# Performance work log

Measured on AMD Instinct MI355X. Metric: run time of the kernel, lower is better.

## Reference

```python
import jax, jax.numpy as jnp
import numpy as np

STATE_DIM = 8
SLOT_DIM = 128
B, T, K = 128, 6, 64


def _mlp(x, w1, b1, w2, b2):
    return jax.nn.relu(x @ w1 + b1) @ w2 + b2


def setup_inputs() -> dict:
    key = jax.random.key(0)
    ks = jax.random.split(key, 24)
    s = 0.02
    def w(k, shape):
        return jax.random.normal(k, shape, dtype=jnp.float32) * s
    D, H = STATE_DIM, SLOT_DIM
    return {
        "gt_states": jax.random.normal(ks[0], (B, T, K, D), dtype=jnp.float32),
        "rollout_steps": 5,
        "enc_w1": w(ks[1], (D, H)),  "enc_b1": jnp.zeros((H,), jnp.float32),
        "enc_w2": w(ks[2], (H, H)),  "enc_b2": jnp.zeros((H,), jnp.float32),
        "self_w1": w(ks[3], (H, H)), "self_b1": jnp.zeros((H,), jnp.float32),
        "self_w2": w(ks[4], (H, H)), "self_b2": jnp.zeros((H,), jnp.float32),
        "inter_w1": w(ks[5], (2 * H, H)), "inter_b1": jnp.zeros((H,), jnp.float32),
        "inter_w2": w(ks[6], (H, H)),     "inter_b2": jnp.zeros((H,), jnp.float32),
        "upd_w1": w(ks[7], (2 * H, H)), "upd_b1": jnp.zeros((H,), jnp.float32),
        "upd_w2": w(ks[8], (H, H)),     "upd_b2": jnp.zeros((H,), jnp.float32),
        "dec_w1": w(ks[9], (H, H)),  "dec_b1": jnp.zeros((H,), jnp.float32),
        "dec_w2": w(ks[10], (H, D)), "dec_b2": jnp.zeros((D,), jnp.float32),
    }


def reference(gt_states, rollout_steps, enc_w1, enc_b1, enc_w2, enc_b2,
              self_w1, self_b1, self_w2, self_b2,
              inter_w1, inter_b1, inter_w2, inter_b2,
              upd_w1, upd_b1, upd_w2, upd_b2,
              dec_w1, dec_b1, dec_w2, dec_b2):
    Tn = gt_states.shape[1]
    n_steps = min(Tn - 1, int(rollout_steps))
    H = enc_w1.shape[1]
    # split the concat-MLP first layer: cat([si, sj]) @ W1 == si @ W1a + sj @ W1b
    wi_a, wi_b = inter_w1[:H], inter_w1[H:]

    slots = _mlp(gt_states[:, 0], enc_w1, enc_b1, enc_w2, enc_b2)  # [B,K,H]
    preds = []
    for _ in range(n_steps):
        delta_self = _mlp(slots, self_w1, self_b1, self_w2, self_b2)  # [B,K,H]
        a = slots @ wi_a  # sender (i) contribution, [B,K,H]
        b = slots @ wi_b  # receiver (j) contribution, [B,K,H]
        # pairwise pre-activation [B,K(i),K(j),H]
        pre = a[:, :, None, :] + b[:, None, :, :] + inter_b1
        effects = jax.nn.relu(pre) @ inter_w2 + inter_b2  # [B,K,K,H]
        delta_inter = effects.mean(axis=1)  # mean over i -> [B,K,H]
        slots = _mlp(jnp.concatenate([delta_self, delta_inter], axis=-1),
                     upd_w1, upd_b1, upd_w2, upd_b2)
        pred = _mlp(slots, dec_w1, dec_b1, dec_w2, dec_b2)  # [B,K,D]
        preds.append(pred)
        slots = _mlp(pred, enc_w1, enc_b1, enc_w2, enc_b2)
    pred_states = jnp.stack(preds, axis=1)  # [B,n_steps,K,D]
    target_states = gt_states[:, 1:int(rollout_steps) + 1]
    return pred_states, target_states
```

## Files before the change

### kernel.cpp

```cpp
#include <hip/hip_runtime.h>

#define BB 128
#define TT 6
#define KK 64
#define DD 8
#define HH 128
#define NSTEP 5
#define LDP 136
#define PREDSZ (BB*NSTEP*KK*DD)

typedef unsigned short u16;
typedef unsigned int   u32;
typedef _Float16 f16;
typedef __attribute__((ext_vector_type(8))) _Float16 f16x8;
typedef __attribute__((ext_vector_type(4))) float f32x4;
typedef __attribute__((ext_vector_type(2))) unsigned int u32x2;
typedef __attribute__((ext_vector_type(4))) unsigned int u32x4;
typedef __attribute__((ext_vector_type(2))) _Float16 h2;

union h2u { u32 u; h2 h; };
union hu  { u16 u; f16 h; };

__device__ __forceinline__ u16 f2h_bits(float f){
  hu v; v.h = (f16)f; return v.u;
}
__device__ __forceinline__ u32 pk2(float x, float y){
  hu a, b; a.h = (f16)x; b.h = (f16)y;
  return (u32)a.u | ((u32)b.u << 16);
}
__device__ __forceinline__ h2 u2h(u32 x){ h2u t; t.u = x; return t.h; }
__device__ __forceinline__ u32 h2u_(h2 x){ h2u t; t.h = x; return t.u; }

#define O_EWA   0
#define O_EWB   16384
#define O_EWS   32768
#define O_SUIU  49152
#define O_UD    81920
#define O_DET   98304
#define O_DW2T  114688
#define BIASF   57856

template<bool RELU>
__device__ __forceinline__ void gemmJ(const u16 (*A)[LDP], const u16* __restrict__ wt,
    float bias, u16 (*O)[LDP], int wn, int wm, int l15, int q, int n, int lane)
{
  f16x8 bf[4];
#pragma unroll
  for (int kc=0; kc<4; ++kc)
    bf[kc] = *(const f16x8*)(wt + (wn<<11) + (kc<<9) + (lane<<3));
#pragma unroll
  for (int mt=0; mt<2; ++mt){
    f32x4 acc = {0.f,0.f,0.f,0.f};
#pragma unroll
    for (int kc=0; kc<4; ++kc){
      f16x8 af = *(const f16x8*)&A[(wm<<5)+(mt<<4)+l15][(kc<<5)+(q<<3)];
      acc = __builtin_amdgcn_mfma_f32_16x16x32_f16(af, bf[kc], acc, 0,0,0);
    }
#pragma unroll
    for (int e=0; e<4; ++e){
      float v = acc[e] + bias;
      if (RELU) v = fmaxf(v, 0.f);
      O[(wm<<5)+(mt<<4)+(q<<2)+e][n] = f2h_bits(v);
    }
  }
}

__device__ __forceinline__ void gemm256J(const u16 (*A1)[LDP], const u16 (*A2)[LDP],
    const u16* __restrict__ wt, float bias, u16 (*O)[LDP], int wn, int wm, int l15, int q, int n, int lane)
{
  f16x8 bf[8];
#pragma unroll
  for (int kc=0; kc<8; ++kc)
    bf[kc] = *(const f16x8*)(wt + (wn<<12) + (kc<<9) + (lane<<3));
#pragma unroll
  for (int mt=0; mt<2; ++mt){
    f32x4 acc = {0.f,0.f,0.f,0.f};
#pragma unroll
    for (int kc=0; kc<8; ++kc){
      const u16 (*As)[LDP] = (kc<4) ? A1 : A2;
      f16x8 af = *(const f16x8*)&As[(wm<<5)+(mt<<4)+l15][((kc&3)<<5)+(q<<3)];
      acc = __builtin_amdgcn_mfma_f32_16x16x32_f16(af, bf[kc], acc, 0,0,0);
    }
#pragma unroll
    for (int e=0; e<4; ++e){
      float v = fmaxf(acc[e] + bias, 0.f);
      O[(wm<<5)+(mt<<4)+(q<<2)+e][n] = f2h_bits(v);
    }
  }
}

__device__ __forceinline__ void fusedS1I(const u16 (*P)[LDP], const u16* __restrict__ ws,
    float bAv, float bBv, float bSv,
    u16 (*Q)[LDP], u16 (*S)[LDP],
    int wn, int wm, int l15, int q, int n, int lane)
{
  f16x8 fa[4], fb[4], fs[4];
#pragma unroll
  for (int kc=0; kc<4; ++kc){
    const int o = (wn<<11) + (kc<<9) + (lane<<3);
    fa[kc] = *(const f16x8*)(ws + O_EWA + o);
    fb[kc] = *(const f16x8*)(ws + O_EWB + o);
    fs[kc] = *(const f16x8*)(ws + O_EWS + o);
  }
  u32 aPk[4][2], bPk[4][2];
#pragma unroll
  for (int mt=0; mt<4; ++mt){
    f16x8 af[4];
#pragma unroll
    for (int kc=0; kc<4; ++kc)
      af[kc] = *(const f16x8*)&P[(mt<<4)+l15][(kc<<5)+(q<<3)];
    f32x4 aA = {0.f,0.f,0.f,0.f}, aB = {0.f,0.f,0.f,0.f};
#pragma unroll
    for (int kc=0; kc<4; ++kc){
      aA = __builtin_amdgcn_mfma_f32_16x16x32_f16(af[kc], fa[kc], aA, 0,0,0);
      aB = __builtin_amdgcn_mfma_f32_16x16x32_f16(af[kc], fb[kc], aB, 0,0,0);
    }
    aPk[mt][0] = pk2(aA[0]+bAv, aA[1]+bAv);
    aPk[mt][1] = pk2(aA[2]+bAv, aA[3]+bAv);
    bPk[mt][0] = pk2(aB[0]+bBv, aB[1]+bBv);
    bPk[mt][1] = pk2(aB[2]+bBv, aB[3]+bBv);
    if ((mt>>1) == wm){
      f32x4 hA = {0.f,0.f,0.f,0.f};
#pragma unroll
      for (int kc=0; kc<4; ++kc)
        hA = __builtin_amdgcn_mfma_f32_16x16x32_f16(af[kc], fs[kc], hA, 0,0,0);
#pragma unroll
      for (int e=0; e<4; ++e)
        S[(mt<<4)+(q<<2)+e][n] = f2h_bits(fmaxf(hA[e]+bSv, 0.f));
    }
  }

  const u32 b0 = bPk[(wm<<1)][0],   b1 = bPk[(wm<<1)][1];
  const u32 b2 = bPk[(wm<<1)+1][0], b3 = bPk[(wm<<1)+1][1];
  u32 jt[4][4];
#pragma unroll
  for (int qp=0; qp<4; ++qp){
    const int src = (qp<<4) + l15;
    jt[qp][0] = (u32)__shfl((int)b0, src);
    jt[qp][1] = (u32)__shfl((int)b1, src);
    jt[qp][2] = (u32)__shfl((int)b2, src);
    jt[qp][3] = (u32)__shfl((int)b3, src);
  }
  h2 z; z.x = (f16)0.f; z.y = (f16)0.f;
  h2 s[4][4];
#pragma unroll
  for (int qp=0; qp<4; ++qp)
#pragma unroll
    for (int X=0; X<4; ++X) s[qp][X] = z;
#pragma unroll
  for (int mt=0; mt<4; ++mt)
#pragma unroll
    for (int p=0; p<2; ++p){
      const u32 ap = aPk[mt][p];
      const h2 hl = u2h(__builtin_amdgcn_perm(ap, ap, 0x01000100));
      const h2 hh = u2h(__builtin_amdgcn_perm(ap, ap, 0x03020302));
#pragma unroll
      for (int qp=0; qp<4; ++qp)
#pragma unroll
        for (int X=0; X<4; ++X){
          const h2 bt = u2h(jt[qp][X]);
          s[qp][X] += __builtin_elementwise_max(hl + bt, z);
          s[qp][X] += __builtin_elementwise_max(hh + bt, z);
        }
    }
#pragma unroll
  for (int m=0; m<2; ++m){
    const int msk = 16 << m;
#pragma unroll
    for (int qp=0; qp<4; ++qp)
#pragma unroll
      for (int X=0; X<4; ++X)
        s[qp][X] += u2h((u32)__shfl_xor((int)h2u_(s[qp][X]), msk));
  }
#pragma unroll
  for (int qp=0; qp<4; ++qp) if (qp == q){
#pragma unroll
    for (int X=0; X<4; ++X){
      const int mh = X>>1, p = X&1;
      const int j = (wm<<5) + (mh<<4) + (qp<<2) + (p<<1);
      hu lo, hi; lo.h = s[qp][X].x; hi.h = s[qp][X].y;
      Q[j][n]   = lo.u;
      Q[j+1][n] = hi.u;
    }
  }
}

__device__ __forceinline__ void dec_out(const u16 (*S)[LDP], const u16* __restrict__ dwt,
    float db2v, float* __restrict__ out, int b, int t, int tid)
{
  const int r = tid>>3, d = tid&7;
  float acc = db2v;
#pragma unroll
  for (int c=0; c<16; ++c){
    f16x8 hv = *(const f16x8*)&S[r][c<<3];
    f16x8 wv = *(const f16x8*)(dwt + (d<<7) + (c<<3));
#pragma unroll
    for (int j=0; j<8; ++j)
      acc += (float)hv[j] * (float)wv[j];
  }
  out[(size_t)(b*NSTEP + t)*(KK*DD) + (r<<3) + d] = acc;
}

__device__ __forceinline__ void mlp_in8(const float* pred, const float* __restrict__ W,
    const float* __restrict__ bias, u16 (*O)[LDP], int tid)
{
  const int h = tid & 127, rg = tid >> 7;
  float wv[DD];
#pragma unroll
  for (int d=0; d<DD; ++d) wv[d] = W[d*HH + h];
  const float bv = bias[h];
  for (int rr=0; rr<8; ++rr){
    const int r = (rg<<3) + rr;
    float v = bv;
#pragma unroll
    for (int d=0; d<DD; ++d) v += pred[r*DD + d] * wv[d];
    O[r][h] = f2h_bits(fmaxf(v, 0.f));
  }
}

__global__ void prep_kernel(
    const float* __restrict__ ew1, const float* __restrict__ eb1,
    const float* __restrict__ ew2, const float* __restrict__ eb2,
    const float* __restrict__ sw1, const float* __restrict__ sb1,
    const float* __restrict__ sw2, const float* __restrict__ sb2,
    const float* __restrict__ iw1, const float* __restrict__ ib1,
    const float* __restrict__ iw2, const float* __restrict__ ib2,
    const float* __restrict__ uw1, const float* __restrict__ ub1,
    const float* __restrict__ uw2, const float* __restrict__ ub2,
    const float* __restrict__ dw1, const float* __restrict__ db1,
    const float* __restrict__ dw2, const float* __restrict__ db2,
    u16* __restrict__ ws)
{
  const int idx = blockIdx.x * 256 + threadIdx.x;
  if (idx < 49152){
    const int mat = idx >> 14, r = idx & 16383;
    const int g = r >> 11, kc = (r >> 9) & 3, lane = (r >> 3) & 63, e = r & 7;
    const int k  = (kc<<5) + ((lane>>4)<<3) + e;
    const int nn = (g<<4) + (lane & 15);
    float v = 0.f;
    if (mat == 0){ for (int m=0; m<HH; ++m) v += ew2[k*HH+m] * iw1[m*HH+nn]; }
    else if (mat == 1){ for (int m=0; m<HH; ++m) v += ew2[k*HH+m] * iw1[(HH+m)*HH+nn]; }
    else { for (int m=0; m<HH; ++m) v += ew2[k*HH+m] * sw1[m*HH+nn]; }
    hu hb; hb.h = (f16)v; ws[idx] = hb.u;
  } else if (idx < 81920){
    const int r = idx - 49152;
    const int g = r >> 12, kc = (r >> 9) & 7, lane = (r >> 3) & 63, e = r & 7;
    const int k  = ((kc&3)<<5) + ((lane>>4)<<3) + e;
    const int nn = (g<<4) + (lane & 15);
    float v = 0.f;
    if (kc < 4){ for (int m=0; m<HH; ++m) v += sw2[k*HH+m] * uw1[m*HH+nn]; }
    else { for (int m=0; m<HH; ++m) v += iw2[k*HH+m] * uw1[(HH+m)*HH+nn]; v *= (1.f/64.f); }
    hu hb; hb.h = (f16)v; ws[idx] = hb.u;
  } else if (idx < 98304){
    const int r = idx - 81920;
    const int g = r >> 11, kc = (r >> 9) & 3, lane = (r >> 3) & 63, e = r & 7;
    const int k  = (kc<<5) + ((lane>>4)<<3) + e;
    const int nn = (g<<4) + (lane & 15);
    float v = 0.f;
    for (int m=0; m<HH; ++m) v += uw2[k*HH+m] * dw1[m*HH+nn];
    hu hb; hb.h = (f16)v; ws[idx] = hb.u;
  } else if (idx < 114688){
    const int r = idx - 98304;
    const int g = r >> 11, kc = (r >> 9) & 3, lane = (r >> 3) & 63, e = r & 7;
    const int k  = (kc<<5) + ((lane>>4)<<3) + e;
    const int nn = (g<<4) + (lane & 15);
    float v = 0.f;
#pragma unroll
    for (int d=0; d<DD; ++d) v += dw2[k*DD+d] * ew1[d*HH+nn];
    hu hb; hb.h = (f16)v; ws[idx] = hb.u;
  } else if (idx < 115712){
    const int r = idx - 114688, d = r >> 7, hcol = r & 127;
    hu hb; hb.h = (f16)dw2[hcol*DD + d]; ws[idx] = hb.u;
  } else if (idx < 116480){
    const int j = idx - 115712, which = j >> 7, nn = j & 127;
    float v = 0.f;
    switch (which){
      case 0: for (int m=0; m<HH; ++m) v += eb2[m] * iw1[m*HH+nn]; break;
      case 1: for (int m=0; m<HH; ++m) v += eb2[m] * iw1[(HH+m)*HH+nn]; v += ib1[nn]; break;
      case 2: for (int m=0; m<HH; ++m) v += eb2[m] * sw1[m*HH+nn]; v += sb1[nn]; break;
      case 3: for (int m=0; m<HH; ++m) v += sb2[m]*uw1[m*HH+nn] + ib2[m]*uw1[(HH+m)*HH+nn];
              v += ub1[nn]; break;
      case 4: for (int m=0; m<HH; ++m) v += ub2[m] * dw1[m*HH+nn]; v += db1[nn]; break;
      default:
#pragma unroll
        for (int d=0; d<DD; ++d) v += db2[d] * ew1[d*HH+nn];
        v += eb1[nn]; break;
    }
    ((float*)ws)[BIASF + j] = v;
  }
}

__global__ __launch_bounds__(1024, 4) void rollout_kernel(
    const float* __restrict__ gt, const int* __restrict__ rollout,
    const float* __restrict__ ew1, const float* __restrict__ eb1,
    const float* __restrict__ db2,
    const u16* __restrict__ ws, float* __restrict__ out)
{
  extern __shared__ u16 smem[];
  u16 (*P)[LDP] = (u16(*)[LDP])smem;
  u16 (*Q)[LDP] = (u16(*)[LDP])(smem + KK*LDP);
  u16 (*R)[LDP] = (u16(*)[LDP])(smem + 2*KK*LDP);
  u16 (*S)[LDP] = (u16(*)[LDP])(smem + 3*KK*LDP);
  float* predbuf = (float*)S;

  const int tid = threadIdx.x, b = blockIdx.x;
  const int w = tid >> 6, lane = tid & 63;
  const int l15 = lane & 15, q = lane >> 4;
  const int wn = w & 7, wm = w >> 3;
  const int n = (wn << 4) + l15;

  int ns = rollout[0];
  if (ns > TT-1) ns = TT-1;
  if (ns > NSTEP) ns = NSTEP;
  if (ns < 0) ns = 0;

  const float* bf32 = (const float*)ws;
  const float bAv  = bf32[BIASF + n];
  const float bBv  = bf32[BIASF + 128 + n];
  const float bSv  = bf32[BIASF + 256 + n];
  const float bUv  = bf32[BIASF + 384 + n];
  const float bUDv = bf32[BIASF + 512 + n];
  const float debv = bf32[BIASF + 640 + n];
  const float db2v = db2[tid & 7];

  for (int i=tid; i<NSTEP*KK*DD; i+=1024)
    out[PREDSZ + b*(NSTEP*KK*DD) + i] = gt[(size_t)b*(TT*KK*DD) + KK*DD + i];
  if (tid < KK*DD) predbuf[tid] = gt[(size_t)b*(TT*KK*DD) + tid];
  __syncthreads();
  mlp_in8(predbuf, ew1, eb1, P, tid);
  __syncthreads();

  for (int t=0; t<ns; ++t){
    fusedS1I(P, ws, bAv, bBv, bSv, Q, S, wn, wm, l15, q, n, lane);
    __syncthreads();
    gemm256J(S, Q, ws+O_SUIU, bUv, R, wn, wm, l15, q, n, lane);
    __syncthreads();
    gemmJ<true>(R, ws+O_UD, bUDv, S, wn, wm, l15, q, n, lane);
    __syncthreads();
    gemmJ<true>(S, ws+O_DET, debv, P, wn, wm, l15, q, n, lane);
    if (tid < 512) dec_out(S, ws+O_DW2T, db2v, out, b, t, tid);
    __syncthreads();
  }
}

extern "C" void kernel_launch(void* const* d_in, const int* in_sizes, int n_in,
                              void* d_out, int out_size, void* d_ws, size_t ws_size,
                              hipStream_t stream)
{
  const float* gt  = (const float*)d_in[0];
  const int*   rs  = (const int*)d_in[1];
  const float* ew1 = (const float*)d_in[2];
  const float* eb1 = (const float*)d_in[3];
  const float* ew2 = (const float*)d_in[4];
  const float* eb2 = (const float*)d_in[5];
  const float* sw1 = (const float*)d_in[6];
  const float* sb1 = (const float*)d_in[7];
  const float* sw2 = (const float*)d_in[8];
  const float* sb2 = (const float*)d_in[9];
  const float* iw1 = (const float*)d_in[10];
  const float* ib1 = (const float*)d_in[11];
  const float* iw2 = (const float*)d_in[12];
  const float* ib2 = (const float*)d_in[13];
  const float* uw1 = (const float*)d_in[14];
  const float* ub1 = (const float*)d_in[15];
  const float* uw2 = (const float*)d_in[16];
  const float* ub2 = (const float*)d_in[17];
  const float* dw1 = (const float*)d_in[18];
  const float* db1 = (const float*)d_in[19];
  const float* dw2 = (const float*)d_in[20];
  const float* db2 = (const float*)d_in[21];
  float* out = (float*)d_out;
  u16*   ws  = (u16*)d_ws;

  const int smem_bytes = 4 * KK * LDP * (int)sizeof(u16);
  (void)hipFuncSetAttribute((const void*)rollout_kernel,
                            hipFuncAttributeMaxDynamicSharedMemorySize, smem_bytes);

  hipLaunchKernelGGL(prep_kernel, dim3(455), dim3(256), 0, stream,
                     ew1, eb1, ew2, eb2, sw1, sb1, sw2, sb2, iw1, ib1, iw2, ib2,
                     uw1, ub1, uw2, ub2, dw1, db1, dw2, db2, ws);
  hipLaunchKernelGGL(rollout_kernel, dim3(BB), dim3(1024), smem_bytes, stream,
                     gt, rs, ew1, eb1, db2, ws, out);
}
```

Baseline: 205.2 us.

## Split each batch across two blocks with global-memory slot exchange per step

Each batch element is now handled by two 512-thread blocks instead of one 1024-thread block, so 256 blocks fill more of the GPU's compute units. Each block computes half the receiver rows and half of the update/decoder rows. After every step the two blocks swap their halves of the new slot matrix through a global workspace buffer, coordinated by release/acquire flags and a spin-wait. This trades more parallelism for an inter-block handshake every step, and both blocks must be co-resident or the wait only ends at the guard limit.

After: 198.3 us. 1.03x faster.

```diff
diff --git a/kernel.cpp b/kernel.cpp
--- a/kernel.cpp
+++ b/kernel.cpp
@@ -39,10 +39,12 @@
 #define O_DET   98304
 #define O_DW2T  114688
 #define BIASF   57856
+#define O_XBUF  131072
+#define O_FLAG  (O_XBUF + 128*2*2*4096)
 
 template<bool RELU>
-__device__ __forceinline__ void gemmJ(const u16 (*A)[LDP], const u16* __restrict__ wt,
-    float bias, u16 (*O)[LDP], int wn, int wm, int l15, int q, int n, int lane)
+__device__ __forceinline__ void gemmH(const u16 (*A)[LDP], const u16* __restrict__ wt,
+    float bias, u16 (*O)[LDP], int wn, int l15, int q, int n, int lane)
 {
   f16x8 bf[4];
 #pragma unroll
@@ -53,20 +55,20 @@
     f32x4 acc = {0.f,0.f,0.f,0.f};
 #pragma unroll
     for (int kc=0; kc<4; ++kc){
-      f16x8 af = *(const f16x8*)&A[(wm<<5)+(mt<<4)+l15][(kc<<5)+(q<<3)];
+      f16x8 af = *(const f16x8*)&A[(mt<<4)+l15][(kc<<5)+(q<<3)];
       acc = __builtin_amdgcn_mfma_f32_16x16x32_f16(af, bf[kc], acc, 0,0,0);
     }
 #pragma unroll
     for (int e=0; e<4; ++e){
       float v = acc[e] + bias;
       if (RELU) v = fmaxf(v, 0.f);
-      O[(wm<<5)+(mt<<4)+(q<<2)+e][n] = f2h_bits(v);
-    }
-  }
-}
-
-__device__ __forceinline__ void gemm256J(const u16 (*A1)[LDP], const u16 (*A2)[LDP],
-    const u16* __restrict__ wt, float bias, u16 (*O)[LDP], int wn, int wm, int l15, int q, int n, int lane)
+      O[(mt<<4)+(q<<2)+e][n] = f2h_bits(v);
+    }
+  }
+}
+
+__device__ __forceinline__ void gemm256H(const u16 (*A1)[LDP], const u16 (*A2)[LDP],
+    const u16* __restrict__ wt, float bias, u16 (*O)[LDP], int wn, int l15, int q, int n, int lane)
 {
   f16x8 bf[8];
 #pragma unroll
@@ -78,13 +80,13 @@
 #pragma unroll
     for (int kc=0; kc<8; ++kc){
       const u16 (*As)[LDP] = (kc<4) ? A1 : A2;
-      f16x8 af = *(const f16x8*)&As[(wm<<5)+(mt<<4)+l15][((kc&3)<<5)+(q<<3)];
+      f16x8 af = *(const f16x8*)&As[(mt<<4)+l15][((kc&3)<<5)+(q<<3)];
       acc = __builtin_amdgcn_mfma_f32_16x16x32_f16(af, bf[kc], acc, 0,0,0);
     }
 #pragma unroll
     for (int e=0; e<4; ++e){
       float v = fmaxf(acc[e] + bias, 0.f);
-      O[(wm<<5)+(mt<<4)+(q<<2)+e][n] = f2h_bits(v);
+      O[(mt<<4)+(q<<2)+e][n] = f2h_bits(v);
     }
   }
 }
@@ -92,7 +94,7 @@
 __device__ __forceinline__ void fusedS1I(const u16 (*P)[LDP], const u16* __restrict__ ws,
     float bAv, float bBv, float bSv,
     u16 (*Q)[LDP], u16 (*S)[LDP],
-    int wn, int wm, int l15, int q, int n, int lane)
+    int wn, int half, int l15, int q, int n, int lane)
 {
   f16x8 fa[4], fb[4], fs[4];
 #pragma unroll
@@ -119,19 +121,19 @@
     aPk[mt][1] = pk2(aA[2]+bAv, aA[3]+bAv);
     bPk[mt][0] = pk2(aB[0]+bBv, aB[1]+bBv);
     bPk[mt][1] = pk2(aB[2]+bBv, aB[3]+bBv);
-    if ((mt>>1) == wm){
+    if ((mt>>1) == half){
       f32x4 hA = {0.f,0.f,0.f,0.f};
 #pragma unroll
       for (int kc=0; kc<4; ++kc)
         hA = __builtin_amdgcn_mfma_f32_16x16x32_f16(af[kc], fs[kc], hA, 0,0,0);
 #pragma unroll
       for (int e=0; e<4; ++e)
-        S[(mt<<4)+(q<<2)+e][n] = f2h_bits(fmaxf(hA[e]+bSv, 0.f));
-    }
-  }
-
-  const u32 b0 = bPk[(wm<<1)][0],   b1 = bPk[(wm<<1)][1];
-  const u32 b2 = bPk[(wm<<1)+1][0], b3 = bPk[(wm<<1)+1][1];
+        S[((mt&1)<<4)+(q<<2)+e][n] = f2h_bits(fmaxf(hA[e]+bSv, 0.f));
+    }
+  }
+
+  const u32 b0 = bPk[(half<<1)][0],   b1 = bPk[(half<<1)][1];
+  const u32 b2 = bPk[(half<<1)+1][0], b3 = bPk[(half<<1)+1][1];
   u32 jt[4][4];
 #pragma unroll
   for (int qp=0; qp<4; ++qp){
@@ -177,7 +179,7 @@
 #pragma unroll
     for (int X=0; X<4; ++X){
       const int mh = X>>1, p = X&1;
-      const int j = (wm<<5) + (mh<<4) + (qp<<2) + (p<<1);
+      const int j = (mh<<4) + (qp<<2) + (p<<1);
       hu lo, hi; lo.h = s[qp][X].x; hi.h = s[qp][X].y;
       Q[j][n]   = lo.u;
       Q[j+1][n] = hi.u;
@@ -186,7 +188,7 @@
 }
 
 __device__ __forceinline__ void dec_out(const u16 (*S)[LDP], const u16* __restrict__ dwt,
-    float db2v, float* __restrict__ out, int b, int t, int tid)
+    float db2v, float* __restrict__ out, int batch, int half, int t, int tid)
 {
   const int r = tid>>3, d = tid&7;
   float acc = db2v;
@@ -198,7 +200,7 @@
     for (int j=0; j<8; ++j)
       acc += (float)hv[j] * (float)wv[j];
   }
-  out[(size_t)(b*NSTEP + t)*(KK*DD) + (r<<3) + d] = acc;
+  out[(size_t)(batch*NSTEP + t)*(KK*DD) + ((half<<5)+r)*DD + d] = acc;
 }
 
 __device__ __forceinline__ void mlp_in8(const float* pred, const float* __restrict__ W,
@@ -209,8 +211,8 @@
 #pragma unroll
   for (int d=0; d<DD; ++d) wv[d] = W[d*HH + h];
   const float bv = bias[h];
-  for (int rr=0; rr<8; ++rr){
-    const int r = (rg<<3) + rr;
+  for (int rr=0; rr<16; ++rr){
+    const int r = (rg<<4) + rr;
     float v = bv;
 #pragma unroll
     for (int d=0; d<DD; ++d) v += pred[r*DD + d] * wv[d];
@@ -232,6 +234,7 @@
     u16* __restrict__ ws)
 {
   const int idx = blockIdx.x * 256 + threadIdx.x;
+  if (idx < 512) ((u32*)(ws + O_FLAG))[idx] = 0;
   if (idx < 49152){
     const int mat = idx >> 14, r = idx & 16383;
     const int g = r >> 11, kc = (r >> 9) & 3, lane = (r >> 3) & 63, e = r & 7;
@@ -290,23 +293,24 @@
   }
 }
 
-__global__ __launch_bounds__(1024, 4) void rollout_kernel(
+__global__ __launch_bounds__(512, 2) void rollout_kernel(
     const float* __restrict__ gt, const int* __restrict__ rollout,
     const float* __restrict__ ew1, const float* __restrict__ eb1,
     const float* __restrict__ db2,
-    const u16* __restrict__ ws, float* __restrict__ out)
+    u16* __restrict__ ws, float* __restrict__ out)
 {
   extern __shared__ u16 smem[];
   u16 (*P)[LDP] = (u16(*)[LDP])smem;
-  u16 (*Q)[LDP] = (u16(*)[LDP])(smem + KK*LDP);
-  u16 (*R)[LDP] = (u16(*)[LDP])(smem + 2*KK*LDP);
-  u16 (*S)[LDP] = (u16(*)[LDP])(smem + 3*KK*LDP);
-  float* predbuf = (float*)S;
-
-  const int tid = threadIdx.x, b = blockIdx.x;
+  u16 (*Q)[LDP] = (u16(*)[LDP])(smem + 64*LDP);
+  u16 (*R)[LDP] = (u16(*)[LDP])(smem + 96*LDP);
+  u16 (*S)[LDP] = (u16(*)[LDP])(smem + 128*LDP);
+  float* predbuf = (float*)Q;
+
+  const int tid = threadIdx.x, blk = blockIdx.x;
+  const int batch = blk & 127, half = blk >> 7;
   const int w = tid >> 6, lane = tid & 63;
   const int l15 = lane & 15, q = lane >> 4;
-  const int wn = w & 7, wm = w >> 3;
+  const int wn = w;
   const int n = (wn << 4) + l15;
 
   int ns = rollout[0];
@@ -323,23 +327,57 @@
   const float debv = bf32[BIASF + 640 + n];
   const float db2v = db2[tid & 7];
 
-  for (int i=tid; i<NSTEP*KK*DD; i+=1024)
-    out[PREDSZ + b*(NSTEP*KK*DD) + i] = gt[(size_t)b*(TT*KK*DD) + KK*DD + i];
-  if (tid < KK*DD) predbuf[tid] = gt[(size_t)b*(TT*KK*DD) + tid];
+  u16* xbuf  = ws + O_XBUF;
+  u32* flags = (u32*)(ws + O_FLAG);
+  const int own  = (batch<<1) + half;
+  const int prt  = (batch<<1) + (1-half);
+
+  for (int i=tid; i<NSTEP*KK*DD/2; i+=512)
+    out[PREDSZ + batch*(NSTEP*KK*DD) + half*(NSTEP*KK*DD/2) + i]
+      = gt[(size_t)batch*(TT*KK*DD) + KK*DD + half*(NSTEP*KK*DD/2) + i];
+  predbuf[tid] = gt[(size_t)batch*(TT*KK*DD) + tid];
   __syncthreads();
   mlp_in8(predbuf, ew1, eb1, P, tid);
   __syncthreads();
 
   for (int t=0; t<ns; ++t){
-    fusedS1I(P, ws, bAv, bBv, bSv, Q, S, wn, wm, l15, q, n, lane);
+    fusedS1I(P, ws, bAv, bBv, bSv, Q, S, wn, half, l15, q, n, lane);
     __syncthreads();
-    gemm256J(S, Q, ws+O_SUIU, bUv, R, wn, wm, l15, q, n, lane);
+    gemm256H(S, Q, ws+O_SUIU, bUv, R, wn, l15, q, n, lane);
     __syncthreads();
-    gemmJ<true>(R, ws+O_UD, bUDv, S, wn, wm, l15, q, n, lane);
+    gemmH<true>(R, ws+O_UD, bUDv, S, wn, l15, q, n, lane);
     __syncthreads();
-    gemmJ<true>(S, ws+O_DET, debv, P, wn, wm, l15, q, n, lane);
-    if (tid < 512) dec_out(S, ws+O_DW2T, db2v, out, b, t, tid);
+    gemmH<true>(S, ws+O_DET, debv, P + (half<<5), wn, l15, q, n, lane);
+    if (tid < 256) dec_out(S, ws+O_DW2T, db2v, out, batch, half, t, tid);
     __syncthreads();
+
+    if (t < ns-1){
+      const int par = t & 1;
+      u16* ob = xbuf + (((own<<1)|par) << 12);
+      {
+        const int r = tid >> 4, c = (tid & 15) << 3;
+        *(f16x8*)(ob + tid*8) = *(const f16x8*)&P[(half<<5)+r][c];
+      }
+      __syncthreads();
+      if (tid == 0){
+        __hip_atomic_store(&flags[(own<<1)|par], (u32)(t+1),
+                           __ATOMIC_RELEASE, __HIP_MEMORY_SCOPE_AGENT);
+        int guard = 0;
+        while (__hip_atomic_load(&flags[(prt<<1)|par],
+                 __ATOMIC_ACQUIRE, __HIP_MEMORY_SCOPE_AGENT) != (u32)(t+1)
+               && guard < (1<<22)){
+          ++guard;
+          __builtin_amdgcn_s_sleep(1);
+        }
+      }
+      __syncthreads();
+      {
+        const u16* pb = xbuf + (((prt<<1)|par) << 12);
+        const int r = tid >> 4, c = (tid & 15) << 3;
+        *(f16x8*)&P[((1-half)<<5)+r][c] = *(const f16x8*)(pb + tid*8);
+      }
+      __syncthreads();
+    }
   }
 }
 
@@ -372,13 +410,13 @@
   float* out = (float*)d_out;
   u16*   ws  = (u16*)d_ws;
 
-  const int smem_bytes = 4 * KK * LDP * (int)sizeof(u16);
+  const int smem_bytes = 160 * LDP * (int)sizeof(u16);
   (void)hipFuncSetAttribute((const void*)rollout_kernel,
                             hipFuncAttributeMaxDynamicSharedMemorySize, smem_bytes);
 
   hipLaunchKernelGGL(prep_kernel, dim3(455), dim3(256), 0, stream,
                      ew1, eb1, ew2, eb2, sw1, sb1, sw2, sb2, iw1, ib1, iw2, ib2,
                      uw1, ub1, uw2, ub2, dw1, db1, dw2, db2, ws);
-  hipLaunchKernelGGL(rollout_kernel, dim3(BB), dim3(1024), smem_bytes, stream,
+  hipLaunchKernelGGL(rollout_kernel, dim3(2*BB), dim3(512), smem_bytes, stream,
                      gt, rs, ew1, eb1, db2, ws, out);
 }
```
